# Kernel optimization log

Measured on AMD Instinct MI355X. Metric: run time of the kernel, lower is better.

Reference implementation:

```python
import jax, jax.numpy as jnp
import numpy as np

BS, IMG, P, GRID, NPATCH = 4, 224, 14, 16, 256
D, HID, NC, NDIST = 384, 2688, 1000, 7
BETA = 0.07
LN_EPS = 1e-6


def setup_inputs() -> dict:
    key = jax.random.key(0)
    ks = jax.random.split(key, 10)
    feat_target = jax.random.normal(ks[0], (BS, NPATCH, D), jnp.float32)
    feat_ref = jax.random.normal(ks[1], (BS, NPATCH, D), jnp.float32)
    labels_ref = jax.random.randint(ks[2], (BS, 1, IMG, IMG), 0, NC, jnp.int32)
    # distractor permutations of the batch (one per distractor sample)
    perms = jnp.argsort(jax.random.uniform(ks[3], (NDIST, BS)), axis=-1).astype(jnp.int32)
    # projector Mlp (fc1 -> GELU -> fc2), xavier-ish scaling
    fc1_w = jax.random.normal(ks[4], (D, HID), jnp.float32) * (1.0 / np.sqrt(D))
    fc1_b = jnp.zeros((HID,), jnp.float32)
    fc2_w = jax.random.normal(ks[5], (HID, D), jnp.float32) * (1.0 / np.sqrt(HID))
    fc2_b = jnp.zeros((D,), jnp.float32)
    ln_w = jnp.ones((D,), jnp.float32)
    ln_b = jnp.zeros((D,), jnp.float32)
    return {"feat_target": feat_target, "feat_ref": feat_ref, "labels_ref": labels_ref,
            "perms": perms, "fc1_w": fc1_w, "fc1_b": fc1_b, "fc2_w": fc2_w,
            "fc2_b": fc2_b, "ln_w": ln_w, "ln_b": ln_b}


def _layer_norm(x, w, b):
    mu = x.mean(-1, keepdims=True)
    var = jnp.mean((x - mu) ** 2, axis=-1, keepdims=True)
    return (x - mu) * jax.lax.rsqrt(var + LN_EPS) * w + b


def _l2norm(x, eps=1e-12):
    n = jnp.sqrt(jnp.sum(x * x, axis=-1, keepdims=True))
    return x / jnp.maximum(n, eps)


def reference(feat_target, feat_ref, labels_ref, perms, fc1_w, fc1_b, fc2_w, fc2_b, ln_w, ln_b):
    bs = feat_target.shape[0]

    def proj_norm(x):
        h = jax.nn.gelu(x @ fc1_w + fc1_b, approximate=False)  # torch nn.GELU (erf)
        return _layer_norm(h @ fc2_w + fc2_b, ln_w, ln_b)

    ft = proj_norm(feat_target)   # (bs, 256, 384)
    fr = proj_norm(feat_ref)      # (bs, 256, 384)

    # patchify ground truth: (bs,1,224,224) -> (bs, 256, 14*14)
    g = labels_ref.reshape(bs, 1, GRID, P, GRID, P).transpose(0, 2, 4, 1, 3, 5)
    g = g.reshape(bs, NPATCH, P * P)
    # per-patch class histogram / (P*P) == one_hot(...).mean(dim=3), without huge one-hot
    seg = (jnp.arange(NPATCH, dtype=jnp.int32)[None, :, None] * NC + g).reshape(bs, -1)
    counts = jax.vmap(lambda s: jax.ops.segment_sum(
        jnp.ones(s.shape, jnp.float32), s, num_segments=NPATCH * NC))(seg)
    label = counts.reshape(bs, NPATCH, NC) / float(P * P)  # (bs, 256, 1000)

    # distractors: block 0 is identity, blocks 1..NDIST are batch permutations
    all_perm = jnp.concatenate([jnp.arange(bs, dtype=perms.dtype)[None], perms], 0)  # (8, bs)
    lab_d = label[all_perm].transpose(1, 0, 2, 3).reshape(bs, -1, NC)   # (bs, 2048, 1000)
    feat_d = fr[all_perm].transpose(1, 0, 2, 3).reshape(bs, -1, D)      # (bs, 2048, 384)

    # cosine-similarity softmax cross attention (soft kNN over labels)
    q = _l2norm(ft)
    k = _l2norm(feat_d)
    attn = jax.nn.softmax(jnp.einsum('bqd,bkd->bqk', q, k) / BETA, axis=-1)
    label_hat = jnp.einsum('bqk,bkc->bqc', attn, lab_d)                 # (bs, 256, 1000)

    label_hat = label_hat.reshape(bs, GRID, GRID, NC).transpose(0, 3, 1, 2)
    # nearest upsample 16x16 -> 224x224 (scale 14 exactly)
    out = jnp.repeat(jnp.repeat(label_hat, P, axis=2), P, axis=3)
    return out
```

## Files before the change

kernel.cpp:

```cpp
#include <hip/hip_runtime.h>

#define BSZ 4
#define NPATCH 256
#define DIM 384
#define HID 2688
#define NCLS 1000
#define KTOT 2048
#define IMGSZ 224
#define PCH 14
#define GRD 16

static constexpr float INV_BETA = 1.0f / 0.07f;
static constexpr float LN_EPS_F = 1e-6f;

typedef unsigned short u16;
typedef unsigned int   u32;
typedef __attribute__((ext_vector_type(8))) __bf16 bf16x8;
typedef __attribute__((ext_vector_type(4))) float  f32x4;

#define WAITVM(n) asm volatile("s_waitcnt vmcnt(" #n ")" ::: "memory")

__device__ __forceinline__ u16 f2bf(float f) {
    u32 u = __float_as_uint(f);
    return (u16)((u + 0x7FFFu + ((u >> 16) & 1u)) >> 16);
}
__device__ __forceinline__ float bf2f(u16 h) {
    return __uint_as_float(((u32)h) << 16);
}
__device__ __forceinline__ f32x4 mfma16(bf16x8 a, bf16x8 b, f32x4 c) {
    return __builtin_amdgcn_mfma_f32_16x16x32_bf16(a, b, c, 0, 0, 0);
}
__device__ __forceinline__ void gll16(const u16* g, u16* l) {
    __builtin_amdgcn_global_load_lds(
        (const __attribute__((address_space(1))) void*)g,
        (__attribute__((address_space(3))) void*)l, 16, 0, 0);
}
__device__ __forceinline__ bf16x8 ld8(const u16* p) {
    return *(const bf16x8*)p;
}
__device__ __forceinline__ int swz(int row, int cseg) {
    return cseg ^ ((row >> 1) & 3);
}

__device__ __forceinline__ void transpose_split_body(
    const float* __restrict__ In, int R, int C, int bx, int by,
    u16* __restrict__ OutHi, u16* __restrict__ OutLo, float (*tile)[33])
{
    int cx = bx * 32, ry = by * 32;
    int t = threadIdx.x;
    int tr = t >> 5, tc = t & 31;
    #pragma unroll
    for (int i = 0; i < 4; ++i)
        tile[tr + i * 8][tc] = In[(size_t)(ry + tr + i * 8) * C + cx + tc];
    __syncthreads();
    int a = t >> 3, seg = t & 7;
    u16 h4[4], l4[4];
    #pragma unroll
    for (int i = 0; i < 4; ++i) {
        float v = tile[seg * 4 + i][a];
        h4[i] = f2bf(v);
        l4[i] = f2bf(v - bf2f(h4[i]));
    }
    size_t off = (size_t)(cx + a) * R + ry + seg * 4;
    *(uint2*)(OutHi + off) = make_uint2((u32)h4[0] | ((u32)h4[1] << 16),
                                        (u32)h4[2] | ((u32)h4[3] << 16));
    *(uint2*)(OutLo + off) = make_uint2((u32)l4[0] | ((u32)l4[1] << 16),
                                        (u32)l4[2] | ((u32)l4[3] << 16));
}

__global__ __launch_bounds__(256) void prep_kernel(
    const float* __restrict__ Xt, const float* __restrict__ Xr,
    const float* __restrict__ fc1w, const float* __restrict__ fc2w,
    const int* __restrict__ labels,
    u16* __restrict__ Xhi, u16* __restrict__ Xlo,
    u16* __restrict__ W1Th, u16* __restrict__ W1Tl,
    u16* __restrict__ W2Th, u16* __restrict__ W2Tl,
    u16* __restrict__ LabT)
{
    __shared__ float tile[32][33];
    __shared__ int hist16[16][NCLS];
    int blk = blockIdx.x, t = threadIdx.x;
    if (blk < 768) {
        int e = (blk * 256 + t) * 4;
        const float* src = (e < 1024 * DIM) ? (Xt + e) : (Xr + e - 1024 * DIM);
        float4 v = *(const float4*)src;
        float x[4] = {v.x, v.y, v.z, v.w};
        u16 h[4], l[4];
        #pragma unroll
        for (int i = 0; i < 4; ++i) {
            h[i] = f2bf(x[i]);
            l[i] = f2bf(x[i] - bf2f(h[i]));
        }
        *(uint2*)(Xhi + e) = make_uint2((u32)h[0] | ((u32)h[1] << 16), (u32)h[2] | ((u32)h[3] << 16));
        *(uint2*)(Xlo + e) = make_uint2((u32)l[0] | ((u32)l[1] << 16), (u32)l[2] | ((u32)l[3] << 16));
    } else if (blk < 1776) {
        int i = blk - 768;
        transpose_split_body(fc1w, DIM, HID, i % (HID / 32), i / (HID / 32), W1Th, W1Tl, tile);
    } else if (blk < 2784) {
        int i = blk - 1776;
        transpose_split_body(fc2w, HID, DIM, i % (DIM / 32), i / (DIM / 32), W2Th, W2Tl, tile);
    } else {
        int bp = blk - 2784;
        int b = bp >> 4, py = bp & 15;
        for (int u = t; u < 16 * NCLS; u += 256) ((int*)hist16)[u] = 0;
        __syncthreads();
        const int* lrow = labels + (size_t)b * IMGSZ * IMGSZ + py * PCH * IMGSZ;
        for (int i = t; i < PCH * IMGSZ; i += 256) {
            int lab = lrow[i];
            int px = (i % IMGSZ) / PCH;
            atomicAdd(&hist16[px][lab], 1);
        }
        __syncthreads();
        const float inv = 1.0f / (PCH * PCH);
        for (int u = t; u < 16 * NCLS; u += 256) {
            int c = u >> 4, px = u & 15;
            LabT[((size_t)(b << 10) + c) * 256 + py * 16 + px] =
                f2bf(hist16[px][c] * inv);
        }
    }
}

template<int MODE>
__global__ __launch_bounds__(256) void gemm64(
    const u16* __restrict__ Ahi, const u16* __restrict__ Alo,
    const u16* __restrict__ Bhi, const u16* __restrict__ Blo,
    const float* __restrict__ bias,
    u16* __restrict__ OutHi, u16* __restrict__ OutLo, float* __restrict__ OutF)
{
    constexpr int K  = (MODE == 1) ? HID : DIM;
    constexpr int KS = (MODE == 1) ? HID / 4 : K;
    constexpr int NT = KS / 32;
    constexpr int N  = (MODE == 0) ? HID : DIM;

    __shared__ u16 As_h[3][128 * 32];
    __shared__ u16 As_l[3][128 * 32];
    __shared__ u16 Bs_h[3][64 * 32];
    __shared__ u16 Bs_l[3][64 * 32];

    const int tid = threadIdx.x, lane = tid & 63, wid = tid >> 6;
    const int wm = wid >> 1, wn = wid & 1;
    int n0, m0;
    if constexpr (MODE == 0) {
        int s = (blockIdx.x & 7) * 84 + (blockIdx.x >> 3);
        n0 = (s % 42) * 64;
        m0 = (s / 42) * 128;
    } else {
        n0 = blockIdx.x * 64;
        m0 = blockIdx.y * 128;
    }

    const u16 *a_h, *a_l, *b_h, *b_l;
    if constexpr (MODE == 0) {
        a_h = Ahi + (size_t)m0 * K;   a_l = Alo + (size_t)m0 * K;
        b_h = Bhi + (size_t)n0 * K;   b_l = Blo + (size_t)n0 * K;
    } else {
        const int kbase = blockIdx.z * KS;
        a_h = Ahi + (size_t)m0 * K + kbase;   a_l = Alo + (size_t)m0 * K + kbase;
        b_h = Bhi + (size_t)n0 * K + kbase;   b_l = Blo + (size_t)n0 * K + kbase;
    }

    auto stage = [&](int buf, int k0) {
        #pragma unroll
        for (int j = 0; j < 2; ++j) {
            int g = j * 256 + tid;
            int row = g >> 2, cs = g & 3;
            int col = swz(row, cs) << 3;
            gll16(a_h + (size_t)row * K + k0 + col, &As_h[buf][g * 8]);
            gll16(a_l + (size_t)row * K + k0 + col, &As_l[buf][g * 8]);
        }
        {
            int row = tid >> 2, cs = tid & 3;
            int col = swz(row, cs) << 3;
            gll16(b_h + (size_t)row * K + k0 + col, &Bs_h[buf][tid * 8]);
            gll16(b_l + (size_t)row * K + k0 + col, &Bs_l[buf][tid * 8]);
        }
    };

    const int l15 = lane & 15, cq = lane >> 4;
    int aoff[4], boff[2];
    #pragma unroll
    for (int i = 0; i < 4; ++i) {
        int ra = wm * 64 + i * 16 + l15;
        aoff[i] = ra * 32 + swz(ra, cq) * 8;
    }
    #pragma unroll
    for (int j = 0; j < 2; ++j) {
        int rb = wn * 32 + j * 16 + l15;
        boff[j] = rb * 32 + swz(rb, cq) * 8;
    }

    f32x4 acc[4][2] = {};

    auto compute = [&](int buf) {
        bf16x8 ah[4], al[4], bh[2], bl[2];
        #pragma unroll
        for (int i = 0; i < 4; ++i) {
            ah[i] = ld8(&As_h[buf][aoff[i]]);
            al[i] = ld8(&As_l[buf][aoff[i]]);
        }
        #pragma unroll
        for (int j = 0; j < 2; ++j) {
            bh[j] = ld8(&Bs_h[buf][boff[j]]);
            bl[j] = ld8(&Bs_l[buf][boff[j]]);
        }
        #pragma unroll
        for (int mi = 0; mi < 4; ++mi)
            #pragma unroll
            for (int ni = 0; ni < 2; ++ni) {
                acc[mi][ni] = mfma16(ah[mi], bh[ni], acc[mi][ni]);
                acc[mi][ni] = mfma16(ah[mi], bl[ni], acc[mi][ni]);
                acc[mi][ni] = mfma16(al[mi], bh[ni], acc[mi][ni]);
            }
    };

    stage(0, 0);
    stage(1, 32);
    int cur = 0;
    for (int t = 0; t < NT - 1; ++t) {
        WAITVM(6);
        __builtin_amdgcn_s_barrier();
        __builtin_amdgcn_sched_barrier(0);
        if (t + 2 < NT) {
            int nb = cur + 2; if (nb >= 3) nb -= 3;
            stage(nb, (t + 2) * 32);
        }
        compute(cur);
        cur = (cur == 2) ? 0 : cur + 1;
    }
    WAITVM(0);
    __builtin_amdgcn_s_barrier();
    __builtin_amdgcn_sched_barrier(0);
    compute(cur);

    #pragma unroll
    for (int mi = 0; mi < 4; ++mi)
        #pragma unroll
        for (int ni = 0; ni < 2; ++ni)
            #pragma unroll
            for (int r = 0; r < 4; ++r) {
                int gm = m0 + wm * 64 + mi * 16 + cq * 4 + r;
                int gn = n0 + wn * 32 + ni * 16 + l15;
                float v = acc[mi][ni][r];
                if constexpr (MODE == 0) {
                    v += bias[gn];
                    v = 0.5f * v * (1.0f + erff(v * 0.7071067811865476f));
                    u16 h = f2bf(v);
                    OutHi[(size_t)gm * N + gn] = h;
                    OutLo[(size_t)gm * N + gn] = f2bf(v - bf2f(h));
                } else {
                    OutF[(size_t)blockIdx.z * (2048 * DIM) + (size_t)gm * N + gn] = v;
                }
            }
}

__global__ __launch_bounds__(256) void qk64(
    const u16* __restrict__ Zhi, const u16* __restrict__ Zlo,
    const int* __restrict__ perms, u16* __restrict__ E)
{
    constexpr int NT = DIM / 32;
    __shared__ u16 As_h[3][64 * 32];
    __shared__ u16 As_l[3][64 * 32];
    __shared__ u16 Bs_h[3][64 * 32];
    __shared__ u16 Bs_l[3][64 * 32];

    const int tid = threadIdx.x, lane = tid & 63, wid = tid >> 6;
    const int wm = wid >> 1, wn = wid & 1;
    const int n0 = blockIdx.x * 64, m0 = blockIdx.y * 64, b = blockIdx.z;
    const int d = n0 >> 8;
    const int apd = (d == 0) ? b : perms[(d - 1) * BSZ + b];

    const u16* a_h = Zhi + (size_t)(b * NPATCH + m0) * DIM;
    const u16* a_l = Zlo + (size_t)(b * NPATCH + m0) * DIM;
    const u16* b_h = Zhi + (size_t)(1024 + apd * NPATCH + (n0 & 255)) * DIM;
    const u16* b_l = Zlo + (size_t)(1024 + apd * NPATCH + (n0 & 255)) * DIM;

    auto stage = [&](int buf, int k0) {
        int row = tid >> 2, cs = tid & 3;
        int col = swz(row, cs) << 3;
        gll16(a_h + (size_t)row * DIM + k0 + col, &As_h[buf][tid * 8]);
        gll16(a_l + (size_t)row * DIM + k0 + col, &As_l[buf][tid * 8]);
        gll16(b_h + (size_t)row * DIM + k0 + col, &Bs_h[buf][tid * 8]);
        gll16(b_l + (size_t)row * DIM + k0 + col, &Bs_l[buf][tid * 8]);
    };

    const int l15 = lane & 15, cq = lane >> 4;
    int aoff[2], boff[2];
    #pragma unroll
    for (int i = 0; i < 2; ++i) {
        int ra = wm * 32 + i * 16 + l15;
        aoff[i] = ra * 32 + swz(ra, cq) * 8;
        int rb = wn * 32 + i * 16 + l15;
        boff[i] = rb * 32 + swz(rb, cq) * 8;
    }

    f32x4 acc[2][2] = {};
    auto compute = [&](int buf) {
        bf16x8 ah[2], al[2], bh[2], bl[2];
        #pragma unroll
        for (int i = 0; i < 2; ++i) {
            ah[i] = ld8(&As_h[buf][aoff[i]]);
            al[i] = ld8(&As_l[buf][aoff[i]]);
            bh[i] = ld8(&Bs_h[buf][boff[i]]);
            bl[i] = ld8(&Bs_l[buf][boff[i]]);
        }
        #pragma unroll
        for (int mi = 0; mi < 2; ++mi)
            #pragma unroll
            for (int ni = 0; ni < 2; ++ni) {
                acc[mi][ni] = mfma16(ah[mi], bh[ni], acc[mi][ni]);
                acc[mi][ni] = mfma16(ah[mi], bl[ni], acc[mi][ni]);
                acc[mi][ni] = mfma16(al[mi], bh[ni], acc[mi][ni]);
            }
    };

    stage(0, 0);
    stage(1, 32);
    int cur = 0;
    for (int t = 0; t < NT - 1; ++t) {
        WAITVM(4);
        __builtin_amdgcn_s_barrier();
        __builtin_amdgcn_sched_barrier(0);
        if (t + 2 < NT) {
            int nb = cur + 2; if (nb >= 3) nb -= 3;
            stage(nb, (t + 2) * 32);
        }
        compute(cur);
        cur = (cur == 2) ? 0 : cur + 1;
    }
    WAITVM(0);
    __builtin_amdgcn_s_barrier();
    __builtin_amdgcn_sched_barrier(0);
    compute(cur);

    #pragma unroll
    for (int mi = 0; mi < 2; ++mi)
        #pragma unroll
        for (int ni = 0; ni < 2; ++ni)
            #pragma unroll
            for (int r = 0; r < 4; ++r) {
                int gm = m0 + wm * 32 + mi * 16 + cq * 4 + r;
                int gn = n0 + wn * 32 + ni * 16 + l15;
                float e = expf((acc[mi][ni][r] - 1.0f) * INV_BETA);
                E[((size_t)b * NPATCH + gm) * KTOT + gn] = f2bf(e);
            }
}

__global__ __launch_bounds__(256) void pv64(
    const u16* __restrict__ E, const u16* __restrict__ LabT,
    const int* __restrict__ perms, float* __restrict__ Lp)
{
    constexpr int KSP = KTOT / 4;
    constexpr int NT  = KSP / 32;
    __shared__ u16 As[3][128 * 32];
    __shared__ u16 Bs[3][64 * 32];

    const int tid = threadIdx.x, lane = tid & 63, wid = tid >> 6;
    const int wm = wid >> 1, wn = wid & 1;
    const int n0 = blockIdx.x * 64, m0 = blockIdx.y * 128;
    const int b = blockIdx.z & 3, ks = blockIdx.z >> 2;
    const int s0 = ks * 2;
    const int apd0 = (s0 == 0) ? b : perms[(s0 - 1) * BSZ + b];
    const int apd1 = perms[s0 * BSZ + b];

    const u16* abase = E + (size_t)(b * NPATCH + m0) * KTOT + ks * KSP;

    auto stage = [&](int buf, int k0) {
        #pragma unroll
        for (int j = 0; j < 2; ++j) {
            int g = j * 256 + tid;
            int row = g >> 2, cs = g & 3;
            int col = swz(row, cs) << 3;
            gll16(abase + (size_t)row * KTOT + k0 + col, &As[buf][g * 8]);
        }
        {
            int apd = (k0 & 256) ? apd1 : apd0;
            int p0 = k0 & 255;
            int row = tid >> 2, cs = tid & 3;
            int col = swz(row, cs) << 3;
            gll16(LabT + ((size_t)(apd << 10) + n0 + row) * 256 + p0 + col,
                  &Bs[buf][tid * 8]);
        }
    };

    const int l15 = lane & 15, cq = lane >> 4;
    int aoff[4], boff[2];
    #pragma unroll
    for (int i = 0; i < 4; ++i) {
        int ra = wm * 64 + i * 16 + l15;
        aoff[i] = ra * 32 + swz(ra, cq) * 8;
    }
    #pragma unroll
    for (int j = 0; j < 2; ++j) {
        int rb = wn * 32 + j * 16 + l15;
        boff[j] = rb * 32 + swz(rb, cq) * 8;
    }

    f32x4 acc[4][2] = {};
    auto compute = [&](int buf) {
        bf16x8 a[4], bb[2];
        #pragma unroll
        for (int i = 0; i < 4; ++i) a[i] = ld8(&As[buf][aoff[i]]);
        #pragma unroll
        for (int j = 0; j < 2; ++j) bb[j] = ld8(&Bs[buf][boff[j]]);
        #pragma unroll
        for (int mi = 0; mi < 4; ++mi)
            #pragma unroll
            for (int ni = 0; ni < 2; ++ni)
                acc[mi][ni] = mfma16(a[mi], bb[ni], acc[mi][ni]);
    };

    stage(0, 0);
    stage(1, 32);
    int cur = 0;
    for (int t = 0; t < NT - 1; ++t) {
        WAITVM(3);
        __builtin_amdgcn_s_barrier();
        __builtin_amdgcn_sched_barrier(0);
        if (t + 2 < NT) {
            int nb = cur + 2; if (nb >= 3) nb -= 3;
            stage(nb, (t + 2) * 32);
        }
        compute(cur);
        cur = (cur == 2) ? 0 : cur + 1;
    }
    WAITVM(0);
    __builtin_amdgcn_s_barrier();
    __builtin_amdgcn_sched_barrier(0);
    compute(cur);

    #pragma unroll
    for (int mi = 0; mi < 4; ++mi)
        #pragma unroll
        for (int ni = 0; ni < 2; ++ni) {
            int gn = n0 + wn * 32 + ni * 16 + l15;
            if (gn < NCLS) {
                #pragma unroll
                for (int r = 0; r < 4; ++r) {
                    int gm = m0 + wm * 64 + mi * 16 + cq * 4 + r;
                    Lp[(((size_t)ks * BSZ + b) * NPATCH + gm) * NCLS + gn] =
                        acc[mi][ni][r];
                }
            }
        }
}

__device__ __forceinline__ float wave_sum(float v) {
    #pragma unroll
    for (int off = 32; off > 0; off >>= 1) v += __shfl_xor(v, off);
    return v;
}

__global__ __launch_bounds__(256) void rowsum_kernel(
    const u16* __restrict__ E, float* __restrict__ R)
{
    int row = blockIdx.x, t = threadIdx.x;
    uint4 u = *(const uint4*)(E + (size_t)row * KTOT + t * 8);
    float s = bf2f(u.x & 0xffff) + bf2f(u.x >> 16)
            + bf2f(u.y & 0xffff) + bf2f(u.y >> 16)
            + bf2f(u.z & 0xffff) + bf2f(u.z >> 16)
            + bf2f(u.w & 0xffff) + bf2f(u.w >> 16);
    s = wave_sum(s);
    __shared__ float red[4];
    if ((t & 63) == 0) red[t >> 6] = s;
    __syncthreads();
    if (t == 0) R[row] = red[0] + red[1] + red[2] + red[3];
}

__global__ __launch_bounds__(256) void ln_l2_kernel(
    const float* __restrict__ P0, const float* __restrict__ fc2b,
    const float* __restrict__ w, const float* __restrict__ b,
    u16* __restrict__ Zhi, u16* __restrict__ Zlo)
{
    const float* P1 = P0 + 1 * 2048 * DIM;
    const float* P2 = P0 + 2 * 2048 * DIM;
    const float* P3 = P0 + 3 * 2048 * DIM;
    int wid = threadIdx.x >> 6, lane = threadIdx.x & 63;
    int row = blockIdx.x * 4 + wid;
    size_t base = (size_t)row * DIM;
    float x[6];
    float s = 0.0f;
    #pragma unroll
    for (int i = 0; i < 6; ++i) {
        int c = lane + 64 * i;
        x[i] = ((P0[base + c] + P1[base + c]) + (P2[base + c] + P3[base + c])) + fc2b[c];
        s += x[i];
    }
    s = wave_sum(s);
    float mu = s * (1.0f / DIM);
    float vs = 0.0f;
    #pragma unroll
    for (int i = 0; i < 6; ++i) { float d = x[i] - mu; vs += d * d; }
    vs = wave_sum(vs);
    float rstd = 1.0f / sqrtf(vs * (1.0f / DIM) + LN_EPS_F);
    float z[6];
    float n2 = 0.0f;
    #pragma unroll
    for (int i = 0; i < 6; ++i) {
        z[i] = (x[i] - mu) * rstd * w[lane + 64 * i] + b[lane + 64 * i];
        n2 += z[i] * z[i];
    }
    n2 = wave_sum(n2);
    float inv = 1.0f / fmaxf(sqrtf(n2), 1e-12f);
    #pragma unroll
    for (int i = 0; i < 6; ++i) {
        float zn = z[i] * inv;
        u16 h = f2bf(zn);
        Zhi[base + lane + 64 * i] = h;
        Zlo[base + lane + 64 * i] = f2bf(zn - bf2f(h));
    }
}

__global__ __launch_bounds__(256) void upsample_kernel(
    const float* __restrict__ Lp, const float* __restrict__ R,
    float* __restrict__ out)
{
    constexpr size_t S = (size_t)BSZ * NPATCH * NCLS;
    int blk = blockIdx.x;
    int gy = blk & 15;
    int bc = blk >> 4;
    int c = bc % NCLS;
    int b = bc / NCLS;
    __shared__ float vals[GRD];
    int t = threadIdx.x;
    if (t < GRD) {
        int q = b * NPATCH + gy * GRD + t;
        size_t i = (size_t)q * NCLS + c;
        vals[t] = ((Lp[i] + Lp[i + S]) + (Lp[i + 2 * S] + Lp[i + 3 * S])) / R[q];
    }
    __syncthreads();
    float* obase = out + ((size_t)(b * NCLS + c) * IMGSZ + gy * PCH) * IMGSZ;
    for (int idx = t; idx < PCH * 56; idx += 256) {
        int x4 = idx % 56, dy = idx / 56;
        int x0 = x4 * 4;
        f32x4 v = {vals[x0 / PCH], vals[(x0 + 1) / PCH],
                   vals[(x0 + 2) / PCH], vals[(x0 + 3) / PCH]};
        __builtin_nontemporal_store(v, (f32x4*)(obase + dy * IMGSZ + x0));
    }
}

extern "C" void kernel_launch(void* const* d_in, const int* in_sizes, int n_in,
                              void* d_out, int out_size, void* d_ws, size_t ws_size,
                              hipStream_t stream)
{
    (void)in_sizes; (void)n_in; (void)out_size; (void)ws_size;
    const float* feat_t = (const float*)d_in[0];
    const float* feat_r = (const float*)d_in[1];
    const int*   labels = (const int*)d_in[2];
    const int*   perms  = (const int*)d_in[3];
    const float* fc1_w  = (const float*)d_in[4];
    const float* fc1_b  = (const float*)d_in[5];
    const float* fc2_w  = (const float*)d_in[6];
    const float* fc2_b  = (const float*)d_in[7];
    const float* ln_w   = (const float*)d_in[8];
    const float* ln_b   = (const float*)d_in[9];
    float* out = (float*)d_out;
    char*  W   = (char*)d_ws;

    u16*   Hhi  = (u16*)(W + 0);
    u16*   Hlo  = (u16*)(W + 11010048);
    u16*   E    = (u16*)(W + 0);
    float* R    = (float*)(W + 4194304);
    float* Lp   = (float*)(W + 4718592);
    float* P0   = (float*)(W + 22020096);
    u16*   Zhi  = (u16*)(W + 34603008);
    u16*   Zlo  = (u16*)(W + 36175872);
    u16*   LabT = (u16*)(W + 37748736);
    u16*   Xhi  = (u16*)(W + 39845888);
    u16*   Xlo  = (u16*)(W + 41418752);
    u16*   W1Th = (u16*)(W + 42991616);
    u16*   W1Tl = (u16*)(W + 45056000);
    u16*   W2Th = (u16*)(W + 47120384);
    u16*   W2Tl = (u16*)(W + 49184768);

    prep_kernel<<<dim3(2848), dim3(256), 0, stream>>>(
        feat_t, feat_r, fc1_w, fc2_w, labels,
        Xhi, Xlo, W1Th, W1Tl, W2Th, W2Tl, LabT);

    gemm64<0><<<dim3(672), dim3(256), 0, stream>>>(
        Xhi, Xlo, W1Th, W1Tl, fc1_b, Hhi, Hlo, nullptr);

    gemm64<1><<<dim3(6, 16, 4), dim3(256), 0, stream>>>(
        Hhi, Hlo, W2Th, W2Tl, nullptr, nullptr, nullptr, P0);

    ln_l2_kernel<<<dim3(2048 / 4), dim3(256), 0, stream>>>(P0, fc2_b, ln_w, ln_b, Zhi, Zlo);

    qk64<<<dim3(32, 4, 4), dim3(256), 0, stream>>>(Zhi, Zlo, perms, E);

    rowsum_kernel<<<dim3(BSZ * NPATCH), dim3(256), 0, stream>>>(E, R);

    pv64<<<dim3(16, 2, 16), dim3(256), 0, stream>>>(E, LabT, perms, Lp);

    upsample_kernel<<<dim3(BSZ * NCLS * GRD), dim3(256), 0, stream>>>(Lp, R, out);
}
```

Measured before the change: 263.8 us.

## Use single bf16 for QK similarity and fuse row sums into QK epilogue

```diff
diff --git a/kernel.cpp b/kernel.cpp
--- a/kernel.cpp
+++ b/kernel.cpp
@@ -254,14 +254,12 @@
 }
 
 __global__ __launch_bounds__(256) void qk64(
-    const u16* __restrict__ Zhi, const u16* __restrict__ Zlo,
-    const int* __restrict__ perms, u16* __restrict__ E)
+    const u16* __restrict__ Z, const int* __restrict__ perms,
+    u16* __restrict__ E, float* __restrict__ R)
 {
     constexpr int NT = DIM / 32;
-    __shared__ u16 As_h[3][64 * 32];
-    __shared__ u16 As_l[3][64 * 32];
-    __shared__ u16 Bs_h[3][64 * 32];
-    __shared__ u16 Bs_l[3][64 * 32];
+    __shared__ u16 As[3][64 * 32];
+    __shared__ u16 Bs[3][64 * 32];
 
     const int tid = threadIdx.x, lane = tid & 63, wid = tid >> 6;
     const int wm = wid >> 1, wn = wid & 1;
@@ -269,18 +267,14 @@
     const int d = n0 >> 8;
     const int apd = (d == 0) ? b : perms[(d - 1) * BSZ + b];
 
-    const u16* a_h = Zhi + (size_t)(b * NPATCH + m0) * DIM;
-    const u16* a_l = Zlo + (size_t)(b * NPATCH + m0) * DIM;
-    const u16* b_h = Zhi + (size_t)(1024 + apd * NPATCH + (n0 & 255)) * DIM;
-    const u16* b_l = Zlo + (size_t)(1024 + apd * NPATCH + (n0 & 255)) * DIM;
+    const u16* a_g = Z + (size_t)(b * NPATCH + m0) * DIM;
+    const u16* b_g = Z + (size_t)(1024 + apd * NPATCH + (n0 & 255)) * DIM;
 
     auto stage = [&](int buf, int k0) {
         int row = tid >> 2, cs = tid & 3;
         int col = swz(row, cs) << 3;
-        gll16(a_h + (size_t)row * DIM + k0 + col, &As_h[buf][tid * 8]);
-        gll16(a_l + (size_t)row * DIM + k0 + col, &As_l[buf][tid * 8]);
-        gll16(b_h + (size_t)row * DIM + k0 + col, &Bs_h[buf][tid * 8]);
-        gll16(b_l + (size_t)row * DIM + k0 + col, &Bs_l[buf][tid * 8]);
+        gll16(a_g + (size_t)row * DIM + k0 + col, &As[buf][tid * 8]);
+        gll16(b_g + (size_t)row * DIM + k0 + col, &Bs[buf][tid * 8]);
     };
 
     const int l15 = lane & 15, cq = lane >> 4;
@@ -295,29 +289,24 @@
 
     f32x4 acc[2][2] = {};
     auto compute = [&](int buf) {
-        bf16x8 ah[2], al[2], bh[2], bl[2];
+        bf16x8 a[2], bb[2];
         #pragma unroll
         for (int i = 0; i < 2; ++i) {
-            ah[i] = ld8(&As_h[buf][aoff[i]]);
-            al[i] = ld8(&As_l[buf][aoff[i]]);
-            bh[i] = ld8(&Bs_h[buf][boff[i]]);
-            bl[i] = ld8(&Bs_l[buf][boff[i]]);
+            a[i] = ld8(&As[buf][aoff[i]]);
+            bb[i] = ld8(&Bs[buf][boff[i]]);
         }
         #pragma unroll
         for (int mi = 0; mi < 2; ++mi)
             #pragma unroll
-            for (int ni = 0; ni < 2; ++ni) {
-                acc[mi][ni] = mfma16(ah[mi], bh[ni], acc[mi][ni]);
-                acc[mi][ni] = mfma16(ah[mi], bl[ni], acc[mi][ni]);
-                acc[mi][ni] = mfma16(al[mi], bh[ni], acc[mi][ni]);
-            }
+            for (int ni = 0; ni < 2; ++ni)
+                acc[mi][ni] = mfma16(a[mi], bb[ni], acc[mi][ni]);
     };
 
     stage(0, 0);
     stage(1, 32);
     int cur = 0;
     for (int t = 0; t < NT - 1; ++t) {
-        WAITVM(4);
+        WAITVM(2);
         __builtin_amdgcn_s_barrier();
         __builtin_amdgcn_sched_barrier(0);
         if (t + 2 < NT) {
@@ -332,6 +321,7 @@
     __builtin_amdgcn_sched_barrier(0);
     compute(cur);
 
+    float rp[2][4] = {};
     #pragma unroll
     for (int mi = 0; mi < 2; ++mi)
         #pragma unroll
@@ -341,8 +331,22 @@
                 int gm = m0 + wm * 32 + mi * 16 + cq * 4 + r;
                 int gn = n0 + wn * 32 + ni * 16 + l15;
                 float e = expf((acc[mi][ni][r] - 1.0f) * INV_BETA);
-                E[((size_t)b * NPATCH + gm) * KTOT + gn] = f2bf(e);
+                u16 h = f2bf(e);
+                E[((size_t)b * NPATCH + gm) * KTOT + gn] = h;
+                rp[mi][r] += bf2f(h);
             }
+    #pragma unroll
+    for (int mi = 0; mi < 2; ++mi)
+        #pragma unroll
+        for (int r = 0; r < 4; ++r) {
+            float v = rp[mi][r];
+            #pragma unroll
+            for (int off = 1; off < 16; off <<= 1) v += __shfl_xor(v, off);
+            if (l15 == 0) {
+                int gm = m0 + wm * 32 + mi * 16 + cq * 4 + r;
+                atomicAdd(&R[(size_t)b * NPATCH + gm], v);
+            }
+        }
 }
 
 __global__ __launch_bounds__(256) void pv64(
@@ -450,26 +454,10 @@
     return v;
 }
 
-__global__ __launch_bounds__(256) void rowsum_kernel(
-    const u16* __restrict__ E, float* __restrict__ R)
-{
-    int row = blockIdx.x, t = threadIdx.x;
-    uint4 u = *(const uint4*)(E + (size_t)row * KTOT + t * 8);
-    float s = bf2f(u.x & 0xffff) + bf2f(u.x >> 16)
-            + bf2f(u.y & 0xffff) + bf2f(u.y >> 16)
-            + bf2f(u.z & 0xffff) + bf2f(u.z >> 16)
-            + bf2f(u.w & 0xffff) + bf2f(u.w >> 16);
-    s = wave_sum(s);
-    __shared__ float red[4];
-    if ((t & 63) == 0) red[t >> 6] = s;
-    __syncthreads();
-    if (t == 0) R[row] = red[0] + red[1] + red[2] + red[3];
-}
-
 __global__ __launch_bounds__(256) void ln_l2_kernel(
     const float* __restrict__ P0, const float* __restrict__ fc2b,
     const float* __restrict__ w, const float* __restrict__ b,
-    u16* __restrict__ Zhi, u16* __restrict__ Zlo)
+    u16* __restrict__ Zbf)
 {
     const float* P1 = P0 + 1 * 2048 * DIM;
     const float* P2 = P0 + 2 * 2048 * DIM;
@@ -502,12 +490,8 @@
     n2 = wave_sum(n2);
     float inv = 1.0f / fmaxf(sqrtf(n2), 1e-12f);
     #pragma unroll
-    for (int i = 0; i < 6; ++i) {
-        float zn = z[i] * inv;
-        u16 h = f2bf(zn);
-        Zhi[base + lane + 64 * i] = h;
-        Zlo[base + lane + 64 * i] = f2bf(zn - bf2f(h));
-    }
+    for (int i = 0; i < 6; ++i)
+        Zbf[base + lane + 64 * i] = f2bf(z[i] * inv);
 }
 
 __global__ __launch_bounds__(256) void upsample_kernel(
@@ -562,8 +546,7 @@
     float* R    = (float*)(W + 4194304);
     float* Lp   = (float*)(W + 4718592);
     float* P0   = (float*)(W + 22020096);
-    u16*   Zhi  = (u16*)(W + 34603008);
-    u16*   Zlo  = (u16*)(W + 36175872);
+    u16*   Zbf  = (u16*)(W + 34603008);
     u16*   LabT = (u16*)(W + 37748736);
     u16*   Xhi  = (u16*)(W + 39845888);
     u16*   Xlo  = (u16*)(W + 41418752);
@@ -582,11 +565,11 @@
     gemm64<1><<<dim3(6, 16, 4), dim3(256), 0, stream>>>(
         Hhi, Hlo, W2Th, W2Tl, nullptr, nullptr, nullptr, P0);
 
-    ln_l2_kernel<<<dim3(2048 / 4), dim3(256), 0, stream>>>(P0, fc2_b, ln_w, ln_b, Zhi, Zlo);
-
-    qk64<<<dim3(32, 4, 4), dim3(256), 0, stream>>>(Zhi, Zlo, perms, E);
-
-    rowsum_kernel<<<dim3(BSZ * NPATCH), dim3(256), 0, stream>>>(E, R);
+    ln_l2_kernel<<<dim3(2048 / 4), dim3(256), 0, stream>>>(P0, fc2_b, ln_w, ln_b, Zbf);
+
+    hipMemsetAsync(R, 0, BSZ * NPATCH * sizeof(float), stream);
+
+    qk64<<<dim3(32, 4, 4), dim3(256), 0, stream>>>(Zbf, perms, E, R);
 
     pv64<<<dim3(16, 2, 16), dim3(256), 0, stream>>>(E, LabT, perms, Lp);
 
```

New measurement: 264.2 us. No clear change (+0.1%).
